# Kernel tuning notes

Hardware: AMD Instinct MI355X
Metric: run time of the kernel (lower is better)

The kernel has to match this reference:

```python
import jax, jax.numpy as jnp
import numpy as np

N_HEAD, D_MODEL, D_K, D_V = 16, 1024, 64, 64
B, S = 2, 2048
LN_EPS = 1e-5


def setup_inputs() -> dict:
    key = jax.random.key(0)
    ks = jax.random.split(key, 9)
    std_qk = np.sqrt(2.0 / (D_MODEL + D_K)).astype(np.float32)
    std_v = np.sqrt(2.0 / (D_MODEL + D_V)).astype(np.float32)
    return {
        "q": jax.random.normal(ks[0], (B, S, D_MODEL), jnp.float32),
        "k": jax.random.normal(ks[1], (B, S, D_MODEL), jnp.float32),
        "v": jax.random.normal(ks[2], (B, S, D_MODEL), jnp.float32),
        # nn.Linear weights stored as [out, in]; we apply x @ W.T
        "w_qs": jax.random.normal(ks[3], (N_HEAD * D_K, D_MODEL), jnp.float32) * std_qk,
        "w_ks": jax.random.normal(ks[4], (N_HEAD * D_K, D_MODEL), jnp.float32) * std_qk,
        "w_vs": jax.random.normal(ks[5], (N_HEAD * D_V, D_MODEL), jnp.float32) * std_v,
        "fc_w": jax.random.normal(ks[6], (D_MODEL, N_HEAD * D_V), jnp.float32) * np.sqrt(2.0 / (D_MODEL + N_HEAD * D_V)).astype(np.float32),
        "fc_b": jnp.zeros((D_MODEL,), jnp.float32),
        "ln_g": jnp.ones((D_MODEL,), jnp.float32),
        "ln_b": jnp.zeros((D_MODEL,), jnp.float32),
    }


def reference(q, k, v, w_qs, w_ks, w_vs, fc_w, fc_b, ln_g, ln_b):
    temperature = jnp.asarray(np.power(D_K, 0.5), q.dtype)
    residual = q
    # projections -> [b, s, h, d]
    qh = (q @ w_qs.T).reshape(B, S, N_HEAD, D_K)
    kh = (k @ w_ks.T).reshape(B, S, N_HEAD, D_K)
    vh = (v @ w_vs.T).reshape(B, S, N_HEAD, D_V)
    # scaled dot-product attention (dropout = identity in eval)
    attn = jnp.einsum('bqhd,bkhd->bhqk', qh, kh) / temperature
    attn = jax.nn.softmax(attn, axis=-1)  # (log_softmax in source is unused)
    out = jnp.einsum('bhqk,bkhd->bqhd', attn, vh).reshape(B, S, N_HEAD * D_V)
    out = out @ fc_w.T + fc_b
    # layer norm over last dim
    x = out + residual
    mu = jnp.mean(x, axis=-1, keepdims=True)
    var = jnp.var(x, axis=-1, keepdims=True)
    return (x - mu) * jax.lax.rsqrt(var + LN_EPS) * ln_g + ln_b
```

## Files before the change

kernel.cpp:

```cpp
#include <hip/hip_runtime.h>
#include <hip/hip_bf16.h>

typedef _Float16 f16x8 __attribute__((ext_vector_type(8)));
typedef _Float16 f16x4 __attribute__((ext_vector_type(4)));
typedef _Float16 f16x2 __attribute__((ext_vector_type(2)));
typedef float f32x4 __attribute__((ext_vector_type(4)));
typedef float f32x16 __attribute__((ext_vector_type(16)));
typedef unsigned u32x4v __attribute__((ext_vector_type(4)));
typedef int i32x2 __attribute__((ext_vector_type(2)));

#define DEVI __device__ __forceinline__

constexpr int S_LEN = 2048;
constexpr int DM    = 1024;
constexpr int NH    = 16;
constexpr int DHD   = 64;
constexpr int MTOT  = 2 * S_LEN;

DEVI f32x4 mfma16(f16x8 a, f16x8 b, f32x4 c) {
    return __builtin_amdgcn_mfma_f32_16x16x32_f16(a, b, c, 0, 0, 0);
}
DEVI f32x16 mfma32(f16x8 a, f16x8 b, f32x16 c) {
    return __builtin_amdgcn_mfma_f32_32x32x16_f16(a, b, c, 0, 0, 0);
}

DEVI f16x2 cvt_pk(float a, float b) {
    return __builtin_bit_cast(f16x2, __builtin_amdgcn_cvt_pkrtz(a, b));
}

DEVI float fexp2(float x) {
#if __has_builtin(__builtin_amdgcn_exp2f)
    return __builtin_amdgcn_exp2f(x);
#else
    return exp2f(x);
#endif
}

DEVI void pl32swap(unsigned &a, unsigned &b) {
#if __has_builtin(__builtin_amdgcn_permlane32_swap)
    i32x2 r = __builtin_bit_cast(i32x2,
        __builtin_amdgcn_permlane32_swap((int)a, (int)b, false, false));
    a = (unsigned)r[0]; b = (unsigned)r[1];
#else
    int idx = (((int)(threadIdx.x & 63)) ^ 32) << 2;
    unsigned ra = (unsigned)__builtin_amdgcn_ds_bpermute(idx, (int)a);
    unsigned rb = (unsigned)__builtin_amdgcn_ds_bpermute(idx, (int)b);
    bool hi = (threadIdx.x & 32) != 0;
    unsigned na = hi ? rb : a;
    unsigned nb = hi ? b  : ra;
    a = na; b = nb;
#endif
}

DEVI void gload_lds16(const _Float16* g, _Float16* l) {
    __builtin_amdgcn_global_load_lds(
        (const __attribute__((address_space(1))) void*)g,
        (__attribute__((address_space(3))) void*)l, 16, 0, 0);
}

__global__ void k_conv(const float* __restrict__ s0, const float* __restrict__ s1,
                       const float* __restrict__ s2, const float* __restrict__ s3,
                       const float* __restrict__ s4, const float* __restrict__ s5,
                       const float* __restrict__ s6,
                       _Float16* __restrict__ d0, _Float16* __restrict__ d1,
                       _Float16* __restrict__ d2, _Float16* __restrict__ d3,
                       _Float16* __restrict__ d4, _Float16* __restrict__ d5,
                       _Float16* __restrict__ d6)
{
    const int QN4 = (MTOT * DM) / 4;
    const int WN4 = (DM * DM) / 4;
    const int TOT = 3 * QN4 + 4 * WN4;
    int stride = gridDim.x * blockDim.x;
    for (int i = blockIdx.x * blockDim.x + threadIdx.x; i < TOT; i += stride) {
        const float* s; _Float16* d; int off;
        if (i < 3 * QN4) {
            int t = i / QN4; off = i - t * QN4;
            s = t == 0 ? s0 : (t == 1 ? s1 : s2);
            d = t == 0 ? d0 : (t == 1 ? d1 : d2);
        } else {
            int j = i - 3 * QN4;
            int t = j / WN4; off = j - t * WN4;
            s = t == 0 ? s3 : (t == 1 ? s4 : (t == 2 ? s5 : s6));
            d = t == 0 ? d3 : (t == 1 ? d4 : (t == 2 ? d5 : d6));
        }
        float4 v = reinterpret_cast<const float4*>(s)[off];
        f16x4 o;
        o[0] = (_Float16)v.x; o[1] = (_Float16)v.y;
        o[2] = (_Float16)v.z; o[3] = (_Float16)v.w;
        *reinterpret_cast<f16x4*>(d + (size_t)off * 4) = o;
    }
}

DEVI void gemm_main(const _Float16* __restrict__ A, const _Float16* __restrict__ Bw,
                    int kLen, int ld, int m0, int n0, f32x4 (&acc)[4][4])
{
    __shared__ __align__(16) _Float16 As[128 * 64];
    __shared__ __align__(16) _Float16 Bs[128 * 64];

    const int tid = threadIdx.x;
    const int lane = tid & 63;
    const int w = tid >> 6;
    const int wm = w >> 1, wn = w & 1;
    const int lrow = lane & 15, lg = lane >> 4;
    const int srow = w * 8 + (lane >> 3);
    const int scol = ((lane & 7) ^ (srow & 7)) * 8;

#pragma unroll
    for (int i = 0; i < 4; i++)
#pragma unroll
        for (int j = 0; j < 4; j++) acc[i][j] = f32x4{0.f, 0.f, 0.f, 0.f};

    const _Float16* gA = A  + (size_t)(m0 + srow) * ld + scol;
    const _Float16* gB = Bw + (size_t)(n0 + srow) * ld + scol;

#pragma unroll
    for (int q = 0; q < 4; q++) {
        gload_lds16(gA + (size_t)q * 32 * ld, &As[(w * 8 + q * 32) * 64]);
        gload_lds16(gB + (size_t)q * 32 * ld, &Bs[(w * 8 + q * 32) * 64]);
    }

    const int kTiles = kLen >> 6;
    for (int kt = 0; kt < kTiles; ++kt) {
        __syncthreads();
#pragma unroll
        for (int kk = 0; kk < 2; kk++) {
            f16x8 af[4], bfm[4];
#pragma unroll
            for (int i = 0; i < 4; i++) {
                int row = wm * 64 + i * 16 + lrow;
                int slot = (kk * 4 + lg) ^ (row & 7);
                af[i] = *reinterpret_cast<const f16x8*>(As + row * 64 + slot * 8);
            }
#pragma unroll
            for (int j = 0; j < 4; j++) {
                int row = wn * 64 + j * 16 + lrow;
                int slot = (kk * 4 + lg) ^ (row & 7);
                bfm[j] = *reinterpret_cast<const f16x8*>(Bs + row * 64 + slot * 8);
            }
#pragma unroll
            for (int i = 0; i < 4; i++)
#pragma unroll
                for (int j = 0; j < 4; j++)
                    acc[i][j] = mfma16(af[i], bfm[j], acc[i][j]);
        }
        if (kt + 1 < kTiles) {
            asm volatile("s_waitcnt lgkmcnt(0)" ::: "memory");
            __builtin_amdgcn_s_barrier();
            const int ko = (kt + 1) * 64;
#pragma unroll
            for (int q = 0; q < 4; q++) {
                gload_lds16(gA + ko + (size_t)q * 32 * ld, &As[(w * 8 + q * 32) * 64]);
                gload_lds16(gB + ko + (size_t)q * 32 * ld, &Bs[(w * 8 + q * 32) * 64]);
            }
        }
    }
}

__global__ __launch_bounds__(256, 4)
void k_proj(const _Float16* __restrict__ qb, const _Float16* __restrict__ kb,
            const _Float16* __restrict__ vb,
            const _Float16* __restrict__ wq, const _Float16* __restrict__ wk,
            const _Float16* __restrict__ wv,
            _Float16* __restrict__ Qh, _Float16* __restrict__ Kh, _Float16* __restrict__ Vt)
{
    const int z = blockIdx.z;
    const _Float16* A = z == 0 ? qb : (z == 1 ? kb : vb);
    const _Float16* B = z == 0 ? wq : (z == 1 ? wk : wv);
    const int m0 = blockIdx.x * 128, n0 = blockIdx.y * 128;
    f32x4 acc[4][4];
    gemm_main(A, B, DM, DM, m0, n0, acc);

    const int lane = threadIdx.x & 63, w = threadIdx.x >> 6;
    const int wm = w >> 1, wn = w & 1;
    const int lrow = lane & 15, lg = lane >> 4;

    if (z < 2) {
        _Float16* O = z == 0 ? Qh : Kh;
        const float scale = (z == 0) ? 0.18033688011112042f : 1.0f;
#pragma unroll
        for (int i = 0; i < 4; i++)
#pragma unroll
            for (int j = 0; j < 4; j++) {
                int n = n0 + wn * 64 + j * 16 + lrow;
                int h = n >> 6, d = n & 63;
#pragma unroll
                for (int r = 0; r < 4; r++) {
                    int m = m0 + wm * 64 + i * 16 + lg * 4 + r;
                    int b = m >> 11, s = m & (S_LEN - 1);
                    size_t idx = ((size_t)(b * NH + h) * S_LEN + s) * DHD + d;
                    O[idx] = (_Float16)(acc[i][j][r] * scale);
                }
            }
    } else {
#pragma unroll
        for (int i = 0; i < 4; i++) {
            int m = m0 + wm * 64 + i * 16 + lg * 4;
            int b = m >> 11, s = m & (S_LEN - 1);
#pragma unroll
            for (int j = 0; j < 4; j++) {
                int n = n0 + wn * 64 + j * 16 + lrow;
                int h = n >> 6, d = n & 63;
                size_t idx = ((size_t)(b * NH + h) * DHD + d) * S_LEN + s;
                f16x4 pk;
#pragma unroll
                for (int r = 0; r < 4; r++) pk[r] = (_Float16)acc[i][j][r];
                *reinterpret_cast<f16x4*>(Vt + idx) = pk;
            }
        }
    }
}

__global__ __launch_bounds__(256, 2)
void k_attn(const _Float16* __restrict__ Q, const _Float16* __restrict__ Kh,
            const _Float16* __restrict__ Vt, _Float16* __restrict__ Ob)
{
    __shared__ __align__(16) _Float16 Kl[2][4096];
    __shared__ __align__(16) _Float16 Vl[2][4096];

    const int tid  = threadIdx.x;
    const int lane = tid & 63, w = tid >> 6;
    const int l31  = lane & 31, hh = lane >> 5;

    const int raw  = blockIdx.x;
    const int swz  = (raw & 7) * 64 + (raw >> 3);
    const int bh   = swz >> 4;
    const int qblk = swz & 15;
    const int q0   = qblk * 128 + w * 32;

    const _Float16* Qb = Q  + (size_t)bh * S_LEN * DHD;
    const _Float16* Kb = Kh + (size_t)bh * S_LEN * DHD;
    const _Float16* Vb = Vt + (size_t)bh * DHD * S_LEN;

    f16x8 qf[4];
#pragma unroll
    for (int step = 0; step < 4; step++)
        qf[step] = *reinterpret_cast<const f16x8*>(
            Qb + (size_t)(q0 + l31) * DHD + step * 16 + hh * 8);

    f32x16 oacc[2], lacc, cinit;
#pragma unroll
    for (int i = 0; i < 16; i++) {
        oacc[0][i] = 0.f; oacc[1][i] = 0.f; lacc[i] = 0.f; cinit[i] = -7.f;
    }
    f16x8 vones;
#pragma unroll
    for (int i = 0; i < 8; i++) vones[i] = (_Float16)1.0f;

    const int sslot = lane >> 3, s3 = lane & 7;
    const _Float16* gK = Kb + (size_t)(w * 16 + s3) * DHD   + sslot * 8;
    const _Float16* gV = Vb + (size_t)(w * 16 + s3) * S_LEN + sslot * 8;
    const int st0 = sslot * 512 + (w * 16 + s3) * 8;

    f16x8 stK[2], stV[2];
#pragma unroll
    for (int i = 0; i < 2; i++) {
        stK[i] = *reinterpret_cast<const f16x8*>(gK + (size_t)i * 8 * DHD);
        stV[i] = *reinterpret_cast<const f16x8*>(gV + (size_t)i * 8 * S_LEN);
    }

    for (int t = 0; t < 32; ++t) {
        const int cur = t & 1;
        _Float16* Kc = Kl[cur];
        _Float16* Vc = Vl[cur];
#pragma unroll
        for (int i = 0; i < 2; i++) {
            *reinterpret_cast<f16x8*>(Kc + st0 + i * 64) = stK[i];
            *reinterpret_cast<f16x8*>(Vc + st0 + i * 64) = stV[i];
        }
        if (t + 1 < 32) {
#pragma unroll
            for (int i = 0; i < 2; i++) {
                stK[i] = *reinterpret_cast<const f16x8*>(gK + (size_t)(t + 1) * 64 * DHD + (size_t)i * 8 * DHD);
                stV[i] = *reinterpret_cast<const f16x8*>(gV + (t + 1) * 64 + (size_t)i * 8 * S_LEN);
            }
        }
        asm volatile("s_waitcnt lgkmcnt(0)" ::: "memory");
        __builtin_amdgcn_s_barrier();

        f32x16 sc0 = cinit, sc1 = cinit;
        __builtin_amdgcn_s_setprio(1);
#pragma unroll
        for (int step = 0; step < 4; step++) {
            const int sl = step * 2 + hh;
            f16x8 ka = *reinterpret_cast<const f16x8*>(Kc + sl * 512 + l31 * 8);
            f16x8 kb = *reinterpret_cast<const f16x8*>(Kc + sl * 512 + 256 + l31 * 8);
            sc0 = mfma32(ka, qf[step], sc0);
            sc1 = mfma32(kb, qf[step], sc1);
        }
        __builtin_amdgcn_s_setprio(0);

#pragma unroll
        for (int kb2 = 0; kb2 < 2; kb2++) {
            const f32x16 sc = kb2 ? sc1 : sc0;
            float e[16];
#pragma unroll
            for (int r = 0; r < 16; r++) e[r] = fexp2(sc[r]);
            unsigned Wa[4], Wb[4];
#pragma unroll
            for (int g = 0; g < 4; g++) {
                Wa[g] = __builtin_bit_cast(unsigned, cvt_pk(e[4 * g],     e[4 * g + 1]));
                Wb[g] = __builtin_bit_cast(unsigned, cvt_pk(e[4 * g + 2], e[4 * g + 3]));
            }
            pl32swap(Wa[0], Wa[1]); pl32swap(Wb[0], Wb[1]);
            pl32swap(Wa[2], Wa[3]); pl32swap(Wb[2], Wb[3]);
#pragma unroll
            for (int win = 0; win < 2; win++) {
                u32x4v fw = {Wa[2 * win], Wb[2 * win], Wa[2 * win + 1], Wb[2 * win + 1]};
                f16x8 pa = __builtin_bit_cast(f16x8, fw);
                const int slotb = kb2 * 4 + win * 2 + hh;
                __builtin_amdgcn_s_setprio(1);
#pragma unroll
                for (int dblk = 0; dblk < 2; dblk++) {
                    f16x8 vf = *reinterpret_cast<const f16x8*>(
                        Vc + slotb * 512 + dblk * 256 + l31 * 8);
                    oacc[dblk] = mfma32(pa, vf, oacc[dblk]);
                }
                lacc = mfma32(pa, vones, lacc);
                __builtin_amdgcn_s_setprio(0);
            }
        }
    }

    const int b = bh >> 4, h = bh & 15;
#pragma unroll
    for (int r = 0; r < 16; r++) {
        const float iq = 1.0f / lacc[r];
        const int qrow = q0 + (r & 3) + 8 * (r >> 2) + 4 * hh;
        const size_t m = (size_t)(b * S_LEN + qrow) * DM + h * 64;
        Ob[m + l31]      = (_Float16)(oacc[0][r] * iq);
        Ob[m + 32 + l31] = (_Float16)(oacc[1][r] * iq);
    }
}

__global__ __launch_bounds__(256, 4)
void k_fc(const _Float16* __restrict__ Ob, const _Float16* __restrict__ Wfc,
          const float* __restrict__ bias,
          _Float16* __restrict__ fcoA, _Float16* __restrict__ fcoB)
{
    const int z = blockIdx.z;
    const int m0 = blockIdx.x * 128, n0 = blockIdx.y * 128;
    f32x4 acc[4][4];
    gemm_main(Ob + z * 512, Wfc + z * 512, 512, DM, m0, n0, acc);

    _Float16* out = z == 0 ? fcoA : fcoB;
    const int lane = threadIdx.x & 63, w = threadIdx.x >> 6;
    const int wm = w >> 1, wn = w & 1;
    const int lrow = lane & 15, lg = lane >> 4;
#pragma unroll
    for (int j = 0; j < 4; j++) {
        int n = n0 + wn * 64 + j * 16 + lrow;
        float bv = (z == 0) ? bias[n] : 0.f;
#pragma unroll
        for (int i = 0; i < 4; i++)
#pragma unroll
            for (int r = 0; r < 4; r++) {
                int m = m0 + wm * 64 + i * 16 + lg * 4 + r;
                out[(size_t)m * DM + n] = (_Float16)(acc[i][j][r] + bv);
            }
    }
}

__global__ void k_ln(const _Float16* __restrict__ fa, const _Float16* __restrict__ fb,
                     const float* __restrict__ res,
                     const float* __restrict__ g, const float* __restrict__ be,
                     float* __restrict__ out)
{
    int row = blockIdx.x * 4 + (threadIdx.x >> 6);
    int lane = threadIdx.x & 63;
    const f16x4* ar = reinterpret_cast<const f16x4*>(fa + (size_t)row * DM);
    const f16x4* br2 = reinterpret_cast<const f16x4*>(fb + (size_t)row * DM);
    const float4* rr = reinterpret_cast<const float4*>(res + (size_t)row * DM);
    float4 v[4];
    float sum = 0.f, sq = 0.f;
#pragma unroll
    for (int t = 0; t < 4; t++) {
        f16x4 a = ar[lane + 64 * t];
        f16x4 bq = br2[lane + 64 * t];
        float4 b = rr[lane + 64 * t];
        float4 c = make_float4((float)a[0] + (float)bq[0] + b.x,
                               (float)a[1] + (float)bq[1] + b.y,
                               (float)a[2] + (float)bq[2] + b.z,
                               (float)a[3] + (float)bq[3] + b.w);
        v[t] = c;
        sum += c.x + c.y + c.z + c.w;
        sq  += c.x * c.x + c.y * c.y + c.z * c.z + c.w * c.w;
    }
#pragma unroll
    for (int o = 1; o < 64; o <<= 1) { sum += __shfl_xor(sum, o); sq += __shfl_xor(sq, o); }
    float mu = sum * (1.f / DM);
    float rstd = rsqrtf(fmaxf(sq * (1.f / DM) - mu * mu, 0.f) + 1e-5f);
    float4* orow = reinterpret_cast<float4*>(out + (size_t)row * DM);
    const float4* gr = reinterpret_cast<const float4*>(g);
    const float4* brr = reinterpret_cast<const float4*>(be);
#pragma unroll
    for (int t = 0; t < 4; t++) {
        float4 gg = gr[lane + 64 * t], bb = brr[lane + 64 * t];
        float4 c = v[t];
        orow[lane + 64 * t] = make_float4((c.x - mu) * rstd * gg.x + bb.x,
                                          (c.y - mu) * rstd * gg.y + bb.y,
                                          (c.z - mu) * rstd * gg.z + bb.z,
                                          (c.w - mu) * rstd * gg.w + bb.w);
    }
}

extern "C" void kernel_launch(void* const* d_in, const int* in_sizes, int n_in,
                              void* d_out, int out_size, void* d_ws, size_t ws_size,
                              hipStream_t stream)
{
    const float* q    = (const float*)d_in[0];
    const float* k    = (const float*)d_in[1];
    const float* v    = (const float*)d_in[2];
    const float* w_qs = (const float*)d_in[3];
    const float* w_ks = (const float*)d_in[4];
    const float* w_vs = (const float*)d_in[5];
    const float* fc_w = (const float*)d_in[6];
    const float* fc_b = (const float*)d_in[7];
    const float* ln_g = (const float*)d_in[8];
    const float* ln_b = (const float*)d_in[9];
    float* out = (float*)d_out;

    if (ws_size < (size_t)67108864) return;

    _Float16* ws  = (_Float16*)d_ws;
    _Float16* qbf = ws;
    _Float16* kbf = qbf + 4194304;
    _Float16* vbf = kbf + 4194304;
    _Float16* wq  = vbf + 4194304;
    _Float16* wk  = wq + 1048576;
    _Float16* wv  = wk + 1048576;
    _Float16* wfc = wv + 1048576;
    _Float16* Qh  = wfc + 1048576;
    _Float16* Kh  = Qh + 4194304;
    _Float16* Vt  = Kh + 4194304;
    _Float16* Ob  = Vt + 4194304;
    _Float16* fcoA = qbf;
    _Float16* fcoB = kbf;

    k_conv<<<2048, 256, 0, stream>>>(q, k, v, w_qs, w_ks, w_vs, fc_w,
                                     qbf, kbf, vbf, wq, wk, wv, wfc);
    k_proj<<<dim3(32, 8, 3), 256, 0, stream>>>(qbf, kbf, vbf, wq, wk, wv, Qh, Kh, Vt);
    k_attn<<<512, 256, 0, stream>>>(Qh, Kh, Vt, Ob);
    k_fc<<<dim3(32, 8, 2), 256, 0, stream>>>(Ob, wfc, fc_b, fcoA, fcoB);
    k_ln<<<1024, 256, 0, stream>>>(fcoA, fcoB, q, ln_g, ln_b, out);
}
```

Before: 124.4 us.

## Pre-swizzle K/V into LDS tile layout and load attention tiles directly to LDS

```diff
diff --git a/kernel.cpp b/kernel.cpp
--- a/kernel.cpp
+++ b/kernel.cpp
@@ -161,7 +161,7 @@
             const _Float16* __restrict__ vb,
             const _Float16* __restrict__ wq, const _Float16* __restrict__ wk,
             const _Float16* __restrict__ wv,
-            _Float16* __restrict__ Qh, _Float16* __restrict__ Kh, _Float16* __restrict__ Vt)
+            _Float16* __restrict__ Qh, _Float16* __restrict__ Ks, _Float16* __restrict__ Vs)
 {
     const int z = blockIdx.z;
     const _Float16* A = z == 0 ? qb : (z == 1 ? kb : vb);
@@ -174,9 +174,8 @@
     const int wm = w >> 1, wn = w & 1;
     const int lrow = lane & 15, lg = lane >> 4;
 
-    if (z < 2) {
-        _Float16* O = z == 0 ? Qh : Kh;
-        const float scale = (z == 0) ? 0.18033688011112042f : 1.0f;
+    if (z == 0) {
+        const float scale = 0.18033688011112042f;
 #pragma unroll
         for (int i = 0; i < 4; i++)
 #pragma unroll
@@ -188,7 +187,24 @@
                     int m = m0 + wm * 64 + i * 16 + lg * 4 + r;
                     int b = m >> 11, s = m & (S_LEN - 1);
                     size_t idx = ((size_t)(b * NH + h) * S_LEN + s) * DHD + d;
-                    O[idx] = (_Float16)(acc[i][j][r] * scale);
+                    Qh[idx] = (_Float16)(acc[i][j][r] * scale);
+                }
+            }
+    } else if (z == 1) {
+#pragma unroll
+        for (int i = 0; i < 4; i++)
+#pragma unroll
+            for (int j = 0; j < 4; j++) {
+                int n = n0 + wn * 64 + j * 16 + lrow;
+                int h = n >> 6, d = n & 63;
+#pragma unroll
+                for (int r = 0; r < 4; r++) {
+                    int m = m0 + wm * 64 + i * 16 + lg * 4 + r;
+                    int b = m >> 11, s = m & (S_LEN - 1);
+                    size_t idx = (size_t)(b * NH + h) * 131072
+                               + (size_t)(s >> 6) * 4096
+                               + (d >> 3) * 512 + (s & 63) * 8 + (d & 7);
+                    Ks[idx] = (_Float16)acc[i][j][r];
                 }
             }
     } else {
@@ -200,19 +216,21 @@
             for (int j = 0; j < 4; j++) {
                 int n = n0 + wn * 64 + j * 16 + lrow;
                 int h = n >> 6, d = n & 63;
-                size_t idx = ((size_t)(b * NH + h) * DHD + d) * S_LEN + s;
+                size_t idx = (size_t)(b * NH + h) * 131072
+                           + (size_t)(s >> 6) * 4096
+                           + ((s >> 3) & 7) * 512 + d * 8 + (s & 7);
                 f16x4 pk;
 #pragma unroll
                 for (int r = 0; r < 4; r++) pk[r] = (_Float16)acc[i][j][r];
-                *reinterpret_cast<f16x4*>(Vt + idx) = pk;
+                *reinterpret_cast<f16x4*>(Vs + idx) = pk;
             }
         }
     }
 }
 
 __global__ __launch_bounds__(256, 2)
-void k_attn(const _Float16* __restrict__ Q, const _Float16* __restrict__ Kh,
-            const _Float16* __restrict__ Vt, _Float16* __restrict__ Ob)
+void k_attn(const _Float16* __restrict__ Q, const _Float16* __restrict__ Ks,
+            const _Float16* __restrict__ Vs, _Float16* __restrict__ Ob)
 {
     __shared__ __align__(16) _Float16 Kl[2][4096];
     __shared__ __align__(16) _Float16 Vl[2][4096];
@@ -228,8 +246,8 @@
     const int q0   = qblk * 128 + w * 32;
 
     const _Float16* Qb = Q  + (size_t)bh * S_LEN * DHD;
-    const _Float16* Kb = Kh + (size_t)bh * S_LEN * DHD;
-    const _Float16* Vb = Vt + (size_t)bh * DHD * S_LEN;
+    const _Float16* gK = Ks + (size_t)bh * 131072 + w * 1024 + lane * 8;
+    const _Float16* gV = Vs + (size_t)bh * 131072 + w * 1024 + lane * 8;
 
     f16x8 qf[4];
 #pragma unroll
@@ -246,36 +264,25 @@
 #pragma unroll
     for (int i = 0; i < 8; i++) vones[i] = (_Float16)1.0f;
 
-    const int sslot = lane >> 3, s3 = lane & 7;
-    const _Float16* gK = Kb + (size_t)(w * 16 + s3) * DHD   + sslot * 8;
-    const _Float16* gV = Vb + (size_t)(w * 16 + s3) * S_LEN + sslot * 8;
-    const int st0 = sslot * 512 + (w * 16 + s3) * 8;
-
-    f16x8 stK[2], stV[2];
 #pragma unroll
     for (int i = 0; i < 2; i++) {
-        stK[i] = *reinterpret_cast<const f16x8*>(gK + (size_t)i * 8 * DHD);
-        stV[i] = *reinterpret_cast<const f16x8*>(gV + (size_t)i * 8 * S_LEN);
+        gload_lds16(gK + i * 512, &Kl[0][w * 1024 + i * 512]);
+        gload_lds16(gV + i * 512, &Vl[0][w * 1024 + i * 512]);
     }
 
     for (int t = 0; t < 32; ++t) {
         const int cur = t & 1;
-        _Float16* Kc = Kl[cur];
-        _Float16* Vc = Vl[cur];
-#pragma unroll
-        for (int i = 0; i < 2; i++) {
-            *reinterpret_cast<f16x8*>(Kc + st0 + i * 64) = stK[i];
-            *reinterpret_cast<f16x8*>(Vc + st0 + i * 64) = stV[i];
-        }
+        asm volatile("s_waitcnt vmcnt(0) lgkmcnt(0)" ::: "memory");
+        __builtin_amdgcn_s_barrier();
         if (t + 1 < 32) {
 #pragma unroll
             for (int i = 0; i < 2; i++) {
-                stK[i] = *reinterpret_cast<const f16x8*>(gK + (size_t)(t + 1) * 64 * DHD + (size_t)i * 8 * DHD);
-                stV[i] = *reinterpret_cast<const f16x8*>(gV + (t + 1) * 64 + (size_t)i * 8 * S_LEN);
-            }
-        }
-        asm volatile("s_waitcnt lgkmcnt(0)" ::: "memory");
-        __builtin_amdgcn_s_barrier();
+                gload_lds16(gK + (t + 1) * 4096 + i * 512, &Kl[cur ^ 1][w * 1024 + i * 512]);
+                gload_lds16(gV + (t + 1) * 4096 + i * 512, &Vl[cur ^ 1][w * 1024 + i * 512]);
+            }
+        }
+        const _Float16* Kc = Kl[cur];
+        const _Float16* Vc = Vl[cur];
 
         f32x16 sc0 = cinit, sc1 = cinit;
         __builtin_amdgcn_s_setprio(1);
@@ -430,16 +437,16 @@
     _Float16* wv  = wk + 1048576;
     _Float16* wfc = wv + 1048576;
     _Float16* Qh  = wfc + 1048576;
-    _Float16* Kh  = Qh + 4194304;
-    _Float16* Vt  = Kh + 4194304;
-    _Float16* Ob  = Vt + 4194304;
+    _Float16* Ks  = Qh + 4194304;
+    _Float16* Vs  = Ks + 4194304;
+    _Float16* Ob  = Vs + 4194304;
     _Float16* fcoA = qbf;
     _Float16* fcoB = kbf;
 
     k_conv<<<2048, 256, 0, stream>>>(q, k, v, w_qs, w_ks, w_vs, fc_w,
                                      qbf, kbf, vbf, wq, wk, wv, wfc);
-    k_proj<<<dim3(32, 8, 3), 256, 0, stream>>>(qbf, kbf, vbf, wq, wk, wv, Qh, Kh, Vt);
-    k_attn<<<512, 256, 0, stream>>>(Qh, Kh, Vt, Ob);
+    k_proj<<<dim3(32, 8, 3), 256, 0, stream>>>(qbf, kbf, vbf, wq, wk, wv, Qh, Ks, Vs);
+    k_attn<<<512, 256, 0, stream>>>(Qh, Ks, Vs, Ob);
     k_fc<<<dim3(32, 8, 2), 256, 0, stream>>>(Ob, wfc, fc_b, fcoA, fcoB);
     k_ln<<<1024, 256, 0, stream>>>(fcoA, fcoB, q, ln_g, ln_b, out);
 }
```

Result: no change. 125.2 us (+0.7%).
